# Kernel optimization log

Hardware: AMD Instinct MI355X
Metric: run time of the kernel (lower is better)

The kernel has to match this reference:

```python
import jax, jax.numpy as jnp
import numpy as np

N_NODES = 100000
N_EDGES = 1600000
N_PAIRS = 500000
IN_C, HID_C, OUT_C = 128, 128, 128


def setup_inputs() -> dict:
    key = jax.random.key(0)
    ks = jax.random.split(key, 12)
    def lin(k, fan_in, shape):
        b = 1.0 / np.sqrt(fan_in)
        return jax.random.uniform(k, shape, jnp.float32, -b, b)
    return {
        "x": jax.random.normal(ks[0], (N_NODES, IN_C), jnp.float32),
        "edge_index": jax.random.randint(ks[1], (2, N_EDGES), 0, N_NODES),
        "edge_pairs": jax.random.randint(ks[2], (2, N_PAIRS), 0, N_NODES),
        "W1": lin(ks[3], IN_C, (IN_C, HID_C)),
        "b1": jnp.zeros((HID_C,), jnp.float32),
        "W2": lin(ks[4], HID_C, (HID_C, OUT_C)),
        "b2": jnp.zeros((OUT_C,), jnp.float32),
        "Wm1": lin(ks[5], 2 * OUT_C, (2 * OUT_C, HID_C)),
        "bm1": lin(ks[6], 2 * OUT_C, (HID_C,)),
        "Wm2": lin(ks[7], HID_C, (HID_C, 1)),
        "bm2": lin(ks[8], HID_C, (1,)),
    }


def reference(x, edge_index, edge_pairs, W1, b1, W2, b2, Wm1, bm1, Wm2, bm2):
    N = x.shape[0]
    loop = jnp.arange(N, dtype=edge_index.dtype)
    row = jnp.concatenate([edge_index[0], loop])  # source nodes (+self loops)
    col = jnp.concatenate([edge_index[1], loop])  # target nodes (+self loops)
    # symmetric GCN normalization: deg^{-1/2}[row] * deg^{-1/2}[col]
    deg = jax.ops.segment_sum(jnp.ones(col.shape, x.dtype), col, num_segments=N)
    dinv = jnp.where(deg > 0, jax.lax.rsqrt(deg), 0.0)
    norm = dinv[row] * dinv[col]  # [E+N]

    def gcn_conv(h, W, b):
        h = h @ W  # transform first (PyG GCNConv lin has no bias)
        msg = h[row] * norm[:, None]
        return jax.ops.segment_sum(msg, col, num_segments=N) + b

    h = jax.nn.relu(gcn_conv(x, W1, b1))
    h = gcn_conv(h, W2, b2)  # dropout p=0.0 -> identity

    src, dst = edge_pairs[0], edge_pairs[1]
    ef = jnp.concatenate([h[src], h[dst]], axis=-1)  # [P, 2*out]
    out = jax.nn.relu(ef @ Wm1 + bm1) @ Wm2 + bm2
    return out.squeeze(-1)
```

## Files before the change

### kernel.cpp

```cpp
#include <hip/hip_runtime.h>
#include <hip/hip_fp16.h>

#define NCH 128
#define G_NODES 256
#define EPB 4096
#define RCAP 4864
#define MAXNB 512
#define KST 40

typedef __attribute__((ext_vector_type(8))) short short8;
typedef _Float16 half8 __attribute__((ext_vector_type(8)));
typedef __attribute__((ext_vector_type(4))) float floatx4;

static inline size_t align256(size_t x){ return (x + 255) & ~(size_t)255; }

__global__ __launch_bounds__(256) void binA_kernel(
    const int* __restrict__ row, const int* __restrict__ col,
    int* __restrict__ gcur, unsigned* __restrict__ bucketed, int E, int NB){
  __shared__ int cnt[MAXNB];
  __shared__ int lbase[MAXNB];
  __shared__ int gbase[MAXNB];
  __shared__ unsigned sorted[EPB];
  __shared__ unsigned short binOf[EPB];
  __shared__ int sh[256];
  __shared__ int carry;
  int t = threadIdx.x;
  int e0 = blockIdx.x * EPB;
  int ecnt = min(EPB, E - e0);
  for (int i = t; i < NB; i += 256) cnt[i] = 0;
  if (t == 0) carry = 0;
  __syncthreads();
  unsigned rec[16]; int bn[16]; int rk[16];
  #pragma unroll
  for (int i = 0; i < 16; i++){
    int e = e0 + i * 256 + t;
    if (e < E){
      int r = row[e], c = col[e];
      bn[i]  = c >> 8;
      rec[i] = (unsigned)r | ((unsigned)(c & 255) << 17);
      rk[i]  = atomicAdd(&cnt[bn[i]], 1);
    } else bn[i] = -1;
  }
  __syncthreads();
  for (int start = 0; start < NB; start += 256){
    int i = start + t;
    int v = (i < NB) ? cnt[i] : 0;
    sh[t] = v; __syncthreads();
    for (int off = 1; off < 256; off <<= 1){
      int val = (t >= off) ? sh[t - off] : 0;
      __syncthreads(); sh[t] += val; __syncthreads();
    }
    if (i < NB) lbase[i] = sh[t] - v + carry;
    __syncthreads();
    if (t == 255) carry += sh[255];
    __syncthreads();
  }
  for (int i = t; i < NB; i += 256){
    int c = cnt[i];
    gbase[i] = (c > 0) ? atomicAdd(&gcur[i], c) : 0;
  }
  __syncthreads();
  #pragma unroll
  for (int i = 0; i < 16; i++){
    if (bn[i] >= 0){
      int pos = lbase[bn[i]] + rk[i];
      sorted[pos] = rec[i];
      binOf[pos]  = (unsigned short)bn[i];
    }
  }
  __syncthreads();
  for (int idx = t; idx < ecnt; idx += 256){
    int b = binOf[idx];
    int gpos = gbase[b] + (idx - lbase[b]);
    if (gpos < RCAP) bucketed[(size_t)b * RCAP + gpos] = sorted[idx];
  }
}

__global__ void wprep_kernel(const float* __restrict__ W1, const float* __restrict__ W2,
                             const float* __restrict__ Wm1, short* __restrict__ planes,
                             int* __restrict__ gcur, int NB){
  if (blockIdx.x < 2){
    int i = blockIdx.x * 256 + threadIdx.x;
    if (i < NB) gcur[i] = 0;
  }
  int mat = blockIdx.x >> 6;
  int idx = ((blockIdx.x & 63) << 8) + threadIdx.x;
  int k = idx >> 7, n = idx & 127;
  const float* src = (mat == 0) ? W1 : (mat == 1) ? W2 : (mat == 2) ? Wm1 : (Wm1 + 16384);
  float x = src[idx];
  short hs, ls;
  if (mat == 0){
    unsigned u = __float_as_uint(x);
    hs = (short)(u >> 16);
    float hf = __uint_as_float(u & 0xFFFF0000u);
    ls = (short)(__float_as_uint(x - hf) >> 16);
  } else {
    __half h = __float2half(x);
    __half l = __float2half(x - __half2float(h));
    hs = __half_as_short(h); ls = __half_as_short(l);
  }
  planes[(size_t)(2 * mat) * 16384 + n * 128 + k]     = hs;
  planes[(size_t)(2 * mat + 1) * 16384 + n * 128 + k] = ls;
}

__global__ __launch_bounds__(512, 3) void fused_gemm_binB(
    const float* __restrict__ X, const short* __restrict__ Whi_,
    const short* __restrict__ Wlo_, __half* __restrict__ O, int nrows, int gemmBlocks,
    const unsigned* __restrict__ bucketed, const int* __restrict__ gcur,
    int* __restrict__ rows_sorted, int* __restrict__ offs,
    int* __restrict__ counts, float* __restrict__ dinv, int N){
  __shared__ __align__(16) char smem[40960];
  int t = threadIdx.x;
  if (blockIdx.x < gemmBlocks){
    short* Xhi = (short*)smem;
    short* Xlo = Xhi + 128 * KST;
    short* Whi = Xlo + 128 * KST;
    short* Wlo = Whi + 128 * KST;
    int w = t >> 6, lane = t & 63;
    int m = lane & 15, q = lane >> 4;
    int row0 = blockIdx.x * 128;
    floatx4 acc[8];
    #pragma unroll
    for (int ct = 0; ct < 8; ct++) acc[ct] = (floatx4)0.f;
    for (int kc = 0; kc < 4; kc++){
      int k0 = kc * 32;
      __syncthreads();
      #pragma unroll
      for (int qq = 0; qq < 2; qq++){
        int f = t + 512 * qq;
        int r = f >> 3, kq = f & 7;
        int gr = row0 + r;
        int grc = (gr < nrows) ? gr : 0;
        float4 v = *(const float4*)(X + (size_t)grc * NCH + k0 + kq * 4);
        short h[4], l[4];
        float vv[4] = {v.x, v.y, v.z, v.w};
        #pragma unroll
        for (int j = 0; j < 4; j++){
          unsigned u = __float_as_uint(vv[j]);
          h[j] = (short)(u >> 16);
          float hf = __uint_as_float(u & 0xFFFF0000u);
          l[j] = (short)(__float_as_uint(vv[j] - hf) >> 16);
        }
        *(uint2*)(Xhi + r * KST + kq * 4) = *(uint2*)h;
        *(uint2*)(Xlo + r * KST + kq * 4) = *(uint2*)l;
      }
      {
        int n = t >> 2, kq = t & 3;
        *(uint4*)(Whi + n * KST + kq * 8) = *(const uint4*)(Whi_ + n * NCH + k0 + kq * 8);
        *(uint4*)(Wlo + n * KST + kq * 8) = *(const uint4*)(Wlo_ + n * NCH + k0 + kq * 8);
      }
      __syncthreads();
      short8 a_hi = *(const short8*)(Xhi + (w * 16 + m) * KST + q * 8);
      short8 a_lo = *(const short8*)(Xlo + (w * 16 + m) * KST + q * 8);
      #pragma unroll
      for (int ct = 0; ct < 8; ct++){
        short8 b_hi = *(const short8*)(Whi + (ct * 16 + m) * KST + q * 8);
        short8 b_lo = *(const short8*)(Wlo + (ct * 16 + m) * KST + q * 8);
        acc[ct] = __builtin_amdgcn_mfma_f32_16x16x32_bf16(a_hi, b_hi, acc[ct], 0, 0, 0);
        acc[ct] = __builtin_amdgcn_mfma_f32_16x16x32_bf16(a_lo, b_hi, acc[ct], 0, 0, 0);
        acc[ct] = __builtin_amdgcn_mfma_f32_16x16x32_bf16(a_hi, b_lo, acc[ct], 0, 0, 0);
      }
    }
    #pragma unroll
    for (int r = 0; r < 4; r++){
      int grow = row0 + w * 16 + q * 4 + r;
      if (grow < nrows){
        #pragma unroll
        for (int ct = 0; ct < 8; ct++)
          O[(size_t)grow * NCH + ct * 16 + m] = __float2half(acc[ct][r]);
      }
    }
  } else {
    int b = blockIdx.x - gemmBlocks;
    unsigned* ledge = (unsigned*)smem;
    int* cnt  = (int*)(smem + RCAP * 4);
    int* cnt2 = cnt + 256;
    int* lex  = cnt2 + 256;
    int* sh   = lex + 256;
    int size = min(gcur[b], RCAP);
    int n0 = b * G_NODES;
    if (t < 256){ cnt[t] = 0; cnt2[t] = 0; }
    __syncthreads();
    for (int i = t; i < size; i += 512){
      unsigned v = bucketed[(size_t)b * RCAP + i];
      ledge[i] = v;
      atomicAdd(&cnt[v >> 17], 1);
    }
    __syncthreads();
    {
      int v = (t < 256) ? cnt[t] : 0;
      if (t < 256) sh[t] = v;
      __syncthreads();
      for (int off = 1; off < 256; off <<= 1){
        int val = (t >= off && t < 256) ? sh[t - off] : 0;
        __syncthreads();
        if (t < 256) sh[t] += val;
        __syncthreads();
      }
      if (t < 256){
        lex[t] = sh[t] - v;
        int n = n0 + t;
        if (n < N){
          counts[n] = v;
          offs[n]   = b * RCAP + sh[t] - v;
          dinv[n]   = rsqrtf((float)v + 1.0f);
        }
      }
    }
    __syncthreads();
    for (int i = t; i < size; i += 512){
      unsigned v = ledge[i];
      int node = v >> 17;
      int pos = lex[node] + atomicAdd(&cnt2[node], 1);
      rows_sorted[(size_t)b * RCAP + pos] = (int)(v & 0x1FFFFu);
    }
  }
}

template<int NCT>
__global__ __launch_bounds__(512, 4) void gemm_f16k(
    const __half* __restrict__ X,
    const short* __restrict__ Whi0, const short* __restrict__ Wlo0,
    const short* __restrict__ Whi1, const short* __restrict__ Wlo1,
    __half* __restrict__ O0, __half* __restrict__ O1, int nrows){
  __shared__ short Xs[128 * KST];
  __shared__ short Whs[NCT * 16 * KST];
  __shared__ short Wls[NCT * 16 * KST];
  int t = threadIdx.x;
  int w = t >> 6, lane = t & 63;
  int m = lane & 15, q = lane >> 4;
  int row0 = blockIdx.x * 128;
  floatx4 acc[NCT];
  #pragma unroll
  for (int ct = 0; ct < NCT; ct++) acc[ct] = (floatx4)0.f;

  for (int kc = 0; kc < 4; kc++){
    int k0 = kc * 32;
    __syncthreads();
    {
      int r = t >> 2, kq = t & 3;
      int gr = row0 + r;
      int grc = (gr < nrows) ? gr : 0;
      *(uint4*)(Xs + r * KST + kq * 8) = *(const uint4*)(X + (size_t)grc * NCH + k0 + kq * 8);
    }
    #pragma unroll
    for (int i = t; i < NCT * 16 * 4; i += 512){
      int n = i >> 2, kq = i & 3;
      const short* sh = (n < 128) ? (Whi0 + n * NCH) : (Whi1 + (n - 128) * NCH);
      const short* sl = (n < 128) ? (Wlo0 + n * NCH) : (Wlo1 + (n - 128) * NCH);
      *(uint4*)(Whs + n * KST + kq * 8) = *(const uint4*)(sh + k0 + kq * 8);
      *(uint4*)(Wls + n * KST + kq * 8) = *(const uint4*)(sl + k0 + kq * 8);
    }
    __syncthreads();
    half8 a = *(const half8*)(Xs + (w * 16 + m) * KST + q * 8);
    #pragma unroll
    for (int ct = 0; ct < NCT; ct++){
      half8 bh = *(const half8*)(Whs + (ct * 16 + m) * KST + q * 8);
      half8 bl = *(const half8*)(Wls + (ct * 16 + m) * KST + q * 8);
      acc[ct] = __builtin_amdgcn_mfma_f32_16x16x32_f16(a, bh, acc[ct], 0, 0, 0);
      acc[ct] = __builtin_amdgcn_mfma_f32_16x16x32_f16(a, bl, acc[ct], 0, 0, 0);
    }
  }
  #pragma unroll
  for (int r = 0; r < 4; r++){
    int grow = row0 + w * 16 + q * 4 + r;
    if (grow < nrows){
      #pragma unroll
      for (int ct = 0; ct < NCT; ct++){
        __half val = __float2half(acc[ct][r]);
        if (ct < 8) O0[(size_t)grow * NCH + ct * 16 + m] = val;
        else        O1[(size_t)grow * NCH + (ct - 8) * 16 + m] = val;
      }
    }
  }
}

__global__ __launch_bounds__(256) void agg_kernel(
    const __half* __restrict__ s, const float* __restrict__ dinv,
    const int* __restrict__ offs, const int* __restrict__ counts,
    const int* __restrict__ rows_sorted, const float* __restrict__ bias,
    __half* __restrict__ outp, int N, int do_relu){
  int wave = (int)((blockIdx.x * blockDim.x + threadIdx.x) >> 6);
  int lane = threadIdx.x & 63;
  if (wave >= N) return;
  int c = wave;
  int g = lane >> 4, h = lane & 15;
  float di = dinv[c];
  float acc[8] = {0.f,0.f,0.f,0.f,0.f,0.f,0.f,0.f};
  if (g == 0){
    uint4 v = *(const uint4*)(s + (size_t)c * NCH + h * 8);
    const __half2* hp = (const __half2*)&v;
    #pragma unroll
    for (int i = 0; i < 4; i++){
      float2 f = __half22float2(hp[i]);
      acc[2*i] = fmaf(di, f.x, acc[2*i]); acc[2*i+1] = fmaf(di, f.y, acc[2*i+1]);
    }
  }
  int off = offs[c], cnt = counts[c];
  for (int chunk = 0; chunk < cnt; chunk += 64){
    int nn = min(64, cnt - chunk);
    int myidx = (lane < nn) ? rows_sorted[off + chunk + lane] : 0;
    float mydinv = (lane < nn) ? dinv[myidx] : 0.f;
    int jmax = (nn + 3) >> 2;
    #pragma unroll 4
    for (int j = 0; j < jmax; j++){
      int e = 4 * j + g;
      int r  = __shfl(myidx, e & 63, 64);
      float dr = __shfl(mydinv, e & 63, 64);
      if (e < nn){
        uint4 v = *(const uint4*)(s + (size_t)r * NCH + h * 8);
        const __half2* hp = (const __half2*)&v;
        #pragma unroll
        for (int i = 0; i < 4; i++){
          float2 f = __half22float2(hp[i]);
          acc[2*i] = fmaf(dr, f.x, acc[2*i]); acc[2*i+1] = fmaf(dr, f.y, acc[2*i+1]);
        }
      }
    }
  }
  #pragma unroll
  for (int i = 0; i < 8; i++){
    acc[i] += __shfl_xor(acc[i], 16, 64);
    acc[i] += __shfl_xor(acc[i], 32, 64);
  }
  if (g == 0){
    float4 b0 = *(const float4*)(bias + h * 8);
    float4 b1 = *(const float4*)(bias + h * 8 + 4);
    float o[8];
    o[0] = di*acc[0]+b0.x; o[1] = di*acc[1]+b0.y; o[2] = di*acc[2]+b0.z; o[3] = di*acc[3]+b0.w;
    o[4] = di*acc[4]+b1.x; o[5] = di*acc[5]+b1.y; o[6] = di*acc[6]+b1.z; o[7] = di*acc[7]+b1.w;
    if (do_relu){
      #pragma unroll
      for (int i = 0; i < 8; i++) o[i] = fmaxf(o[i], 0.f);
    }
    __half2 packed[4];
    #pragma unroll
    for (int i = 0; i < 4; i++) packed[i] = __floats2half2_rn(o[2*i], o[2*i+1]);
    *(uint4*)(outp + (size_t)c * NCH + h * 8) = *(uint4*)packed;
  }
}

__global__ __launch_bounds__(256) void pair_kernel(
    const __half* __restrict__ A, const __half* __restrict__ B,
    const int* __restrict__ src, const int* __restrict__ dst,
    const float* __restrict__ bm1, const float* __restrict__ Wm2,
    const float* __restrict__ bm2, float* __restrict__ outp, int P){
  int gwave = (int)((blockIdx.x * blockDim.x + threadIdx.x) >> 6);
  int lane  = threadIdx.x & 63;
  int nw    = (int)((gridDim.x * blockDim.x) >> 6);
  int g = lane >> 4, h = lane & 15;
  float bb[8], ww[8];
  {
    float4 t0 = *(const float4*)(bm1 + h * 8);
    float4 t1 = *(const float4*)(bm1 + h * 8 + 4);
    bb[0]=t0.x; bb[1]=t0.y; bb[2]=t0.z; bb[3]=t0.w;
    bb[4]=t1.x; bb[5]=t1.y; bb[6]=t1.z; bb[7]=t1.w;
    float4 w0 = *(const float4*)(Wm2 + h * 8);
    float4 w1 = *(const float4*)(Wm2 + h * 8 + 4);
    ww[0]=w0.x; ww[1]=w0.y; ww[2]=w0.z; ww[3]=w0.w;
    ww[4]=w1.x; ww[5]=w1.y; ww[6]=w1.z; ww[7]=w1.w;
  }
  float bsc = bm2[0];
  const __half* basep = (g & 1) ? B : A;
  for (int p0 = gwave * 2; p0 < P; p0 += nw * 2){
    int pi = p0 + (g >> 1);
    int piX = (pi < P) ? pi : p0;
    int node = (g & 1) ? dst[piX] : src[piX];
    uint4 v = *(const uint4*)(basep + (size_t)node * NCH + h * 8);
    const __half2* hp = (const __half2*)&v;
    float f[8];
    #pragma unroll
    for (int i = 0; i < 4; i++){
      float2 t2 = __half22float2(hp[i]);
      f[2*i] = t2.x; f[2*i+1] = t2.y;
    }
    float partial = 0.f;
    #pragma unroll
    for (int i = 0; i < 8; i++){
      float other = __shfl_xor(f[i], 16, 64);
      float zi = fmaxf(f[i] + other + bb[i], 0.f);
      partial += zi * ww[i];
    }
    partial += __shfl_xor(partial, 1, 64);
    partial += __shfl_xor(partial, 2, 64);
    partial += __shfl_xor(partial, 4, 64);
    partial += __shfl_xor(partial, 8, 64);
    if ((lane & 31) == 0 && pi < P) outp[pi] = partial + bsc;
  }
}


extern "C" void kernel_launch(void* const* d_in, const int* in_sizes, int n_in,
                              void* d_out, int out_size, void* d_ws, size_t ws_size,
                              hipStream_t stream){
  const float* x   = (const float*)d_in[0];
  const int*   ei  = (const int*)  d_in[1];
  const int*   ep  = (const int*)  d_in[2];
  const float* W1  = (const float*)d_in[3];
  const float* b1  = (const float*)d_in[4];
  const float* W2  = (const float*)d_in[5];
  const float* b2  = (const float*)d_in[6];
  const float* Wm1 = (const float*)d_in[7];
  const float* bm1 = (const float*)d_in[8];
  const float* Wm2 = (const float*)d_in[9];
  const float* bm2 = (const float*)d_in[10];
  float* outp = (float*)d_out;

  const int N = in_sizes[0] / NCH;
  const int E = in_sizes[1] / 2;
  const int P = in_sizes[2] / 2;
  const int NB = (N + G_NODES - 1) / G_NODES;

  char* base = (char*)d_ws;
  size_t off = 0;
  int*      counts      = (int*)     (base + off); off = align256(off + (size_t)N * 4);
  int*      offs        = (int*)     (base + off); off = align256(off + (size_t)N * 4);
  float*    dinv        = (float*)   (base + off); off = align256(off + (size_t)N * 4);
  int*      gcur        = (int*)     (base + off); off = align256(off + (size_t)NB * 4);
  unsigned* bucketed    = (unsigned*)(base + off); off = align256(off + (size_t)NB * RCAP * 4);
  int*      rows_sorted = (int*)     (base + off); off = align256(off + (size_t)NB * RCAP * 4);
  short*    planes      = (short*)   (base + off); off = align256(off + (size_t)8 * 16384 * 2);
  __half*   s1buf       = (__half*)  (base + off); off = align256(off + (size_t)N * NCH * 2);
  __half*   h1buf       = (__half*)  (base + off); off = align256(off + (size_t)N * NCH * 2);
  __half*   s2buf       = (__half*)  (base + off); off = align256(off + (size_t)N * NCH * 2);
  __half*   sA          = (__half*)  (base + off); off = align256(off + (size_t)N * NCH * 2);
  __half*   sB          = (__half*)  (base + off); off = align256(off + (size_t)N * NCH * 2);
  (void)ws_size; (void)n_in; (void)out_size;

  short* W1hi = planes + 0 * 16384;
  short* W1lo = planes + 1 * 16384;
  short* W2hi = planes + 2 * 16384;
  short* W2lo = planes + 3 * 16384;
  short* Wahi = planes + 4 * 16384;
  short* Walo = planes + 5 * 16384;
  short* Wbhi = planes + 6 * 16384;
  short* Wblo = planes + 7 * 16384;

  const int* row = ei;
  const int* col = ei + E;
  const int* psrc = ep;
  const int* pdst = ep + P;

  int gemm_grid = (N + 127) / 128;
  int agg_grid  = (N + 3) / 4;

  wprep_kernel<<<256, 256, 0, stream>>>(W1, W2, Wm1, planes, gcur, NB);
  binA_kernel<<<(E + EPB - 1) / EPB, 256, 0, stream>>>(row, col, gcur, bucketed, E, NB);
  fused_gemm_binB<<<gemm_grid + NB, 512, 0, stream>>>(
      x, W1hi, W1lo, s1buf, N, gemm_grid,
      bucketed, gcur, rows_sorted, offs, counts, dinv, N);
  agg_kernel<<<agg_grid, 256, 0, stream>>>(s1buf, dinv, offs, counts, rows_sorted, b1, h1buf, N, 1);
  gemm_f16k<8><<<gemm_grid, 512, 0, stream>>>(h1buf, W2hi, W2lo, W2hi, W2lo, s2buf, s2buf, N);
  agg_kernel<<<agg_grid, 256, 0, stream>>>(s2buf, dinv, offs, counts, rows_sorted, b2, h1buf, N, 0);
  gemm_f16k<16><<<gemm_grid, 512, 0, stream>>>(h1buf, Wahi, Walo, Wbhi, Wblo, sA, sB, N);
  pair_kernel<<<8192, 256, 0, stream>>>(sA, sB, psrc, pdst, bm1, Wm2, bm2, outp, P);
}
```

Baseline: 395.3 us.

## Fold source dinv into GEMM epilogue, merge weight prep, double pair ILP

```diff
diff --git a/kernel.cpp b/kernel.cpp
--- a/kernel.cpp
+++ b/kernel.cpp
@@ -16,7 +16,9 @@
 
 __global__ __launch_bounds__(256) void binA_kernel(
     const int* __restrict__ row, const int* __restrict__ col,
-    int* __restrict__ gcur, unsigned* __restrict__ bucketed, int E, int NB){
+    int* __restrict__ gcur, unsigned* __restrict__ bucketed, int E, int NB,
+    const float* __restrict__ W1, const float* __restrict__ W2,
+    const float* __restrict__ Wm1, short* __restrict__ planes){
   __shared__ int cnt[MAXNB];
   __shared__ int lbase[MAXNB];
   __shared__ int gbase[MAXNB];
@@ -74,36 +76,32 @@
     int gpos = gbase[b] + (idx - lbase[b]);
     if (gpos < RCAP) bucketed[(size_t)b * RCAP + gpos] = sorted[idx];
   }
-}
-
-__global__ void wprep_kernel(const float* __restrict__ W1, const float* __restrict__ W2,
-                             const float* __restrict__ Wm1, short* __restrict__ planes,
-                             int* __restrict__ gcur, int NB){
-  if (blockIdx.x < 2){
-    int i = blockIdx.x * 256 + threadIdx.x;
-    if (i < NB) gcur[i] = 0;
-  }
-  int mat = blockIdx.x >> 6;
-  int idx = ((blockIdx.x & 63) << 8) + threadIdx.x;
-  int k = idx >> 7, n = idx & 127;
-  const float* src = (mat == 0) ? W1 : (mat == 1) ? W2 : (mat == 2) ? Wm1 : (Wm1 + 16384);
-  float x = src[idx];
-  short hs, ls;
-  if (mat == 0){
-    unsigned u = __float_as_uint(x);
-    hs = (short)(u >> 16);
-    float hf = __uint_as_float(u & 0xFFFF0000u);
-    ls = (short)(__float_as_uint(x - hf) >> 16);
-  } else {
-    __half h = __float2half(x);
-    __half l = __float2half(x - __half2float(h));
-    hs = __half_as_short(h); ls = __half_as_short(l);
-  }
-  planes[(size_t)(2 * mat) * 16384 + n * 128 + k]     = hs;
-  planes[(size_t)(2 * mat + 1) * 16384 + n * 128 + k] = ls;
-}
-
-__global__ __launch_bounds__(512, 3) void fused_gemm_binB(
+  {
+    int gid = blockIdx.x * 256 + t;
+    if (gid < 4 * 16384){
+      int mat = gid >> 14;
+      int idx = gid & 16383;
+      int k = idx >> 7, n = idx & 127;
+      const float* src = (mat == 0) ? W1 : (mat == 1) ? W2 : (mat == 2) ? Wm1 : (Wm1 + 16384);
+      float x = src[idx];
+      short hs, ls;
+      if (mat == 0){
+        unsigned u = __float_as_uint(x);
+        hs = (short)(u >> 16);
+        float hf = __uint_as_float(u & 0xFFFF0000u);
+        ls = (short)(__float_as_uint(x - hf) >> 16);
+      } else {
+        __half h = __float2half(x);
+        __half l = __float2half(x - __half2float(h));
+        hs = __half_as_short(h); ls = __half_as_short(l);
+      }
+      planes[(size_t)(2 * mat) * 16384 + n * 128 + k]     = hs;
+      planes[(size_t)(2 * mat + 1) * 16384 + n * 128 + k] = ls;
+    }
+  }
+}
+
+__global__ __launch_bounds__(512, 4) void fused_gemm_binB(
     const float* __restrict__ X, const short* __restrict__ Whi_,
     const short* __restrict__ Wlo_, __half* __restrict__ O, int nrows, int gemmBlocks,
     const unsigned* __restrict__ bucketed, const int* __restrict__ gcur,
@@ -222,6 +220,7 @@
     const __half* __restrict__ X,
     const short* __restrict__ Whi0, const short* __restrict__ Wlo0,
     const short* __restrict__ Whi1, const short* __restrict__ Wlo1,
+    const float* __restrict__ scale, int do_scale,
     __half* __restrict__ O0, __half* __restrict__ O1, int nrows){
   __shared__ short Xs[128 * KST];
   __shared__ short Whs[NCT * 16 * KST];
@@ -265,9 +264,10 @@
   for (int r = 0; r < 4; r++){
     int grow = row0 + w * 16 + q * 4 + r;
     if (grow < nrows){
+      float sc = do_scale ? scale[grow] : 1.0f;
       #pragma unroll
       for (int ct = 0; ct < NCT; ct++){
-        __half val = __float2half(acc[ct][r]);
+        __half val = __float2half(acc[ct][r] * sc);
         if (ct < 8) O0[(size_t)grow * NCH + ct * 16 + m] = val;
         else        O1[(size_t)grow * NCH + (ct - 8) * 16 + m] = val;
       }
@@ -279,13 +279,14 @@
     const __half* __restrict__ s, const float* __restrict__ dinv,
     const int* __restrict__ offs, const int* __restrict__ counts,
     const int* __restrict__ rows_sorted, const float* __restrict__ bias,
-    __half* __restrict__ outp, int N, int do_relu){
+    __half* __restrict__ outp, int N, int do_relu, int edge_dinv){
   int wave = (int)((blockIdx.x * blockDim.x + threadIdx.x) >> 6);
   int lane = threadIdx.x & 63;
   if (wave >= N) return;
   int c = wave;
   int g = lane >> 4, h = lane & 15;
   float di = dinv[c];
+  float wself = edge_dinv ? di : 1.0f;
   float acc[8] = {0.f,0.f,0.f,0.f,0.f,0.f,0.f,0.f};
   if (g == 0){
     uint4 v = *(const uint4*)(s + (size_t)c * NCH + h * 8);
@@ -293,20 +294,21 @@
     #pragma unroll
     for (int i = 0; i < 4; i++){
       float2 f = __half22float2(hp[i]);
-      acc[2*i] = fmaf(di, f.x, acc[2*i]); acc[2*i+1] = fmaf(di, f.y, acc[2*i+1]);
+      acc[2*i] = fmaf(wself, f.x, acc[2*i]); acc[2*i+1] = fmaf(wself, f.y, acc[2*i+1]);
     }
   }
   int off = offs[c], cnt = counts[c];
   for (int chunk = 0; chunk < cnt; chunk += 64){
     int nn = min(64, cnt - chunk);
     int myidx = (lane < nn) ? rows_sorted[off + chunk + lane] : 0;
-    float mydinv = (lane < nn) ? dinv[myidx] : 0.f;
+    float mydinv = 1.0f;
+    if (edge_dinv && lane < nn) mydinv = dinv[myidx];
     int jmax = (nn + 3) >> 2;
     #pragma unroll 4
     for (int j = 0; j < jmax; j++){
       int e = 4 * j + g;
       int r  = __shfl(myidx, e & 63, 64);
-      float dr = __shfl(mydinv, e & 63, 64);
+      float dr = edge_dinv ? __shfl(mydinv, e & 63, 64) : 1.0f;
       if (e < nn){
         uint4 v = *(const uint4*)(s + (size_t)r * NCH + h * 8);
         const __half2* hp = (const __half2*)&v;
@@ -362,30 +364,45 @@
   }
   float bsc = bm2[0];
   const __half* basep = (g & 1) ? B : A;
-  for (int p0 = gwave * 2; p0 < P; p0 += nw * 2){
-    int pi = p0 + (g >> 1);
-    int piX = (pi < P) ? pi : p0;
-    int node = (g & 1) ? dst[piX] : src[piX];
-    uint4 v = *(const uint4*)(basep + (size_t)node * NCH + h * 8);
-    const __half2* hp = (const __half2*)&v;
-    float f[8];
+  const int* idxp = (g & 1) ? dst : src;
+  for (int p0 = gwave * 4; p0 < P; p0 += nw * 4){
+    int piA = p0 + (g >> 1);
+    int piB = p0 + 2 + (g >> 1);
+    int piAX = (piA < P) ? piA : P - 1;
+    int piBX = (piB < P) ? piB : P - 1;
+    int nodeA = idxp[piAX];
+    int nodeB = idxp[piBX];
+    uint4 vA = *(const uint4*)(basep + (size_t)nodeA * NCH + h * 8);
+    uint4 vB = *(const uint4*)(basep + (size_t)nodeB * NCH + h * 8);
+    const __half2* hpA = (const __half2*)&vA;
+    const __half2* hpB = (const __half2*)&vB;
+    float fA[8], fB[8];
     #pragma unroll
     for (int i = 0; i < 4; i++){
-      float2 t2 = __half22float2(hp[i]);
-      f[2*i] = t2.x; f[2*i+1] = t2.y;
-    }
-    float partial = 0.f;
+      float2 ta = __half22float2(hpA[i]);
+      float2 tb = __half22float2(hpB[i]);
+      fA[2*i] = ta.x; fA[2*i+1] = ta.y;
+      fB[2*i] = tb.x; fB[2*i+1] = tb.y;
+    }
+    float pA = 0.f, pB = 0.f;
     #pragma unroll
     for (int i = 0; i < 8; i++){
-      float other = __shfl_xor(f[i], 16, 64);
-      float zi = fmaxf(f[i] + other + bb[i], 0.f);
-      partial += zi * ww[i];
-    }
-    partial += __shfl_xor(partial, 1, 64);
-    partial += __shfl_xor(partial, 2, 64);
-    partial += __shfl_xor(partial, 4, 64);
-    partial += __shfl_xor(partial, 8, 64);
-    if ((lane & 31) == 0 && pi < P) outp[pi] = partial + bsc;
+      float oA = __shfl_xor(fA[i], 16, 64);
+      float oB = __shfl_xor(fB[i], 16, 64);
+      float zA = fmaxf(fA[i] + oA + bb[i], 0.f);
+      float zB = fmaxf(fB[i] + oB + bb[i], 0.f);
+      pA += zA * ww[i];
+      pB += zB * ww[i];
+    }
+    #pragma unroll
+    for (int d = 1; d <= 8; d <<= 1){
+      pA += __shfl_xor(pA, d, 64);
+      pB += __shfl_xor(pB, d, 64);
+    }
+    if ((lane & 31) == 0){
+      if (piA < P) outp[piA] = pA + bsc;
+      if (piB < P) outp[piB] = pB + bsc;
+    }
   }
 }
 
@@ -444,14 +461,15 @@
   int gemm_grid = (N + 127) / 128;
   int agg_grid  = (N + 3) / 4;
 
-  wprep_kernel<<<256, 256, 0, stream>>>(W1, W2, Wm1, planes, gcur, NB);
-  binA_kernel<<<(E + EPB - 1) / EPB, 256, 0, stream>>>(row, col, gcur, bucketed, E, NB);
+  hipMemsetAsync(gcur, 0, (size_t)NB * 4, stream);
+  binA_kernel<<<(E + EPB - 1) / EPB, 256, 0, stream>>>(row, col, gcur, bucketed, E, NB,
+                                                       W1, W2, Wm1, planes);
   fused_gemm_binB<<<gemm_grid + NB, 512, 0, stream>>>(
       x, W1hi, W1lo, s1buf, N, gemm_grid,
       bucketed, gcur, rows_sorted, offs, counts, dinv, N);
-  agg_kernel<<<agg_grid, 256, 0, stream>>>(s1buf, dinv, offs, counts, rows_sorted, b1, h1buf, N, 1);
-  gemm_f16k<8><<<gemm_grid, 512, 0, stream>>>(h1buf, W2hi, W2lo, W2hi, W2lo, s2buf, s2buf, N);
-  agg_kernel<<<agg_grid, 256, 0, stream>>>(s2buf, dinv, offs, counts, rows_sorted, b2, h1buf, N, 0);
-  gemm_f16k<16><<<gemm_grid, 512, 0, stream>>>(h1buf, Wahi, Walo, Wbhi, Wblo, sA, sB, N);
+  agg_kernel<<<agg_grid, 256, 0, stream>>>(s1buf, dinv, offs, counts, rows_sorted, b1, h1buf, N, 1, 1);
+  gemm_f16k<8><<<gemm_grid, 512, 0, stream>>>(h1buf, W2hi, W2lo, W2hi, W2lo, dinv, 1, s2buf, s2buf, N);
+  agg_kernel<<<agg_grid, 256, 0, stream>>>(s2buf, dinv, offs, counts, rows_sorted, b2, h1buf, N, 0, 0);
+  gemm_f16k<16><<<gemm_grid, 512, 0, stream>>>(h1buf, Wahi, Walo, Wbhi, Wblo, dinv, 0, sA, sB, N);
   pair_kernel<<<8192, 256, 0, stream>>>(sA, sB, psrc, pdst, bm1, Wm2, bm2, outp, P);
 }
```

After: 382.8 us. 1.03x faster.
